# Performance work log

Hardware: AMD Instinct MI355X
Metric: run time of the kernel (lower is better)

The kernel has to match this reference:

```python
import jax, jax.numpy as jnp
import numpy as np

N, DEG, F_IN, F_OUT = 100000, 16, 128, 128
E = N * DEG


def setup_inputs() -> dict:
    key = jax.random.key(0)
    k0, k1, k2, k3 = jax.random.split(key, 4)
    x = jax.random.normal(k0, (N, F_IN), dtype=jnp.float32)
    # ragged neighbor list flattened: each node has DEG neighbors (sorted segment ids)
    neighbor_feats = jax.random.normal(k1, (E, F_IN), dtype=jnp.float32)
    segment_ids = jnp.repeat(jnp.arange(N, dtype=jnp.int32), DEG)
    # nn.Linear(in, out, bias=False) weights, stored [out, in] as in torch
    Wx = jax.random.normal(k2, (F_OUT, F_IN), dtype=jnp.float32) / np.float32(np.sqrt(F_IN))
    Wn = jax.random.normal(k3, (F_OUT, F_IN), dtype=jnp.float32) / np.float32(np.sqrt(F_IN))
    return {"x": x, "neighbor_feats": neighbor_feats, "segment_ids": segment_ids,
            "Wx": Wx, "Wn": Wn}


def reference(x, neighbor_feats, segment_ids, Wx, Wn):
    n_nodes = x.shape[0]
    # MeanAggregator: per-node mean over its neighbor rows (segment mean)
    sums = jax.ops.segment_sum(neighbor_feats, segment_ids, num_segments=n_nodes)
    counts = jax.ops.segment_sum(
        jnp.ones((neighbor_feats.shape[0],), dtype=x.dtype), segment_ids,
        num_segments=n_nodes)
    f = sums / jnp.maximum(counts, 1.0)[:, None]  # [N, F_IN]
    # tranx(x) + trann(f)
    x_out = x @ Wx.T + f @ Wn.T                   # [N, F_OUT]
    # neighbor = [tranx(n) for n in neighbor], flattened
    nb_out = neighbor_feats @ Wx.T                # [E, F_OUT]
    return x_out, nb_out
```

## Files before the change

kernel.cpp:

```cpp
#include <hip/hip_runtime.h>
#include <stdint.h>
#include <stddef.h>

#define N_NODES 100000
#define F_DIM   128
#define DEG     16
#define N_EDGES (N_NODES*DEG)
#define ROWS_PER_TILE 128
#define N_TILES (N_EDGES/ROWS_PER_TILE)
#define NODES_PER_TILE (ROWS_PER_TILE/DEG)
#define GRID_BLOCKS 2500
#define TILES_PER_BLOCK (N_TILES/GRID_BLOCKS)
#define BLOCK_THREADS 256
#define G_STRIDE 132

typedef __bf16 bf16;
typedef __bf16 bf16x8 __attribute__((ext_vector_type(8)));
typedef float  f32x4  __attribute__((ext_vector_type(4)));

__device__ __forceinline__ int swz(int row, int col) {
  return row*128 + (col ^ ((row & 7) << 3));
}

__device__ __forceinline__ bf16x8 cvt8(f32x4 a, f32x4 b) {
  bf16x8 v;
  v[0]=(bf16)a[0]; v[1]=(bf16)a[1]; v[2]=(bf16)a[2]; v[3]=(bf16)a[3];
  v[4]=(bf16)b[0]; v[5]=(bf16)b[1]; v[6]=(bf16)b[2]; v[7]=(bf16)b[3];
  return v;
}

__device__ __forceinline__ bf16x8 load_frag_g(const float* __restrict__ p) {
  f32x4 a = *(const f32x4*)p;
  f32x4 b = *(const f32x4*)(p + 4);
  return cvt8(a, b);
}

__global__ __launch_bounds__(BLOCK_THREADS, 2)
void feattrans_kernel(const float* __restrict__ x,
                      const float* __restrict__ nb,
                      const float* __restrict__ Wx,
                      const float* __restrict__ Wn,
                      float* __restrict__ out)
{
  __shared__ bf16  w_lds[2*128*128];
  __shared__ float g_lds[2][NODES_PER_TILE][G_STRIDE];

  const int tid  = threadIdx.x;
  const int wave = tid >> 6;
  const int lane = tid & 63;
  const int l15  = lane & 15;
  const int lk   = lane >> 4;

  #pragma unroll
  for (int it = 0; it < 16; ++it) {
    int idx = it * BLOCK_THREADS + tid;
    int mat = idx >> 11;
    int rem = idx & 2047;
    int row = rem >> 4;
    int g   = rem & 15;
    const float* src = (mat ? Wn : Wx) + row*128 + g*8;
    bf16x8 v = load_frag_g(src);
    *(bf16x8*)&w_lds[mat*16384 + swz(row, g*8)] = v;
  }
  __syncthreads();

  float* out_x  = out;
  float* out_nb = out + (size_t)N_NODES * F_DIM;

  const int bid = blockIdx.x;

  bf16x8 afr[2][2][4];

  {
    const size_t erow0 = (size_t)bid * ROWS_PER_TILE;
    #pragma unroll
    for (int mt = 0; mt < 2; ++mt)
      #pragma unroll
      for (int ks = 0; ks < 4; ++ks)
        afr[0][mt][ks] = load_frag_g(nb + (erow0 + wave*32 + mt*16 + l15) * F_DIM + ks*32 + lk*8);
  }

  #pragma unroll
  for (int t = 0; t < TILES_PER_BLOCK; ++t) {
    const int cur = t & 1, nxt = cur ^ 1;
    const int tile = bid + t * GRID_BLOCKS;
    const size_t erow0 = (size_t)tile * ROWS_PER_TILE;
    const int nodebase = tile * NODES_PER_TILE;

    int xrow = nodebase + l15;
    if (xrow > N_NODES - 1) xrow = N_NODES - 1;
    bf16x8 xfr[4];
    #pragma unroll
    for (int ks = 0; ks < 4; ++ks)
      xfr[ks] = load_frag_g(x + (size_t)xrow * F_DIM + ks*32 + lk*8);

    f32x4 acc[2][8] = {};
    #pragma unroll
    for (int nt = 0; nt < 8; ++nt) {
      #pragma unroll
      for (int ks = 0; ks < 4; ++ks) {
        bf16x8 bfr = *(bf16x8*)&w_lds[swz(nt*16 + l15, ks*32 + lk*8)];
        acc[0][nt] = __builtin_amdgcn_mfma_f32_16x16x32_bf16(bfr, afr[cur][0][ks], acc[0][nt], 0, 0, 0);
        acc[1][nt] = __builtin_amdgcn_mfma_f32_16x16x32_bf16(bfr, afr[cur][1][ks], acc[1][nt], 0, 0, 0);
      }
    }
    #pragma unroll
    for (int mt = 0; mt < 2; ++mt)
      #pragma unroll
      for (int nt = 0; nt < 8; ++nt)
        *(f32x4*)(out_nb + (erow0 + wave*32 + mt*16 + l15) * F_DIM + nt*16 + lk*4) = acc[mt][nt];

    f32x4 a2[2][8] = {};
    #pragma unroll
    for (int nt = 0; nt < 8; ++nt) {
      #pragma unroll
      for (int ks = 0; ks < 4; ++ks) {
        bf16x8 bfr = *(bf16x8*)&w_lds[16384 + swz(nt*16 + l15, ks*32 + lk*8)];
        a2[0][nt] = __builtin_amdgcn_mfma_f32_16x16x32_bf16(afr[cur][0][ks], bfr, a2[0][nt], 0, 0, 0);
        a2[1][nt] = __builtin_amdgcn_mfma_f32_16x16x32_bf16(afr[cur][1][ks], bfr, a2[1][nt], 0, 0, 0);
      }
    }
    #pragma unroll
    for (int mt = 0; mt < 2; ++mt) {
      const int gnode = 2*wave + mt;
      #pragma unroll
      for (int nt = 0; nt < 8; ++nt) {
        float s = a2[mt][nt][0] + a2[mt][nt][1] + a2[mt][nt][2] + a2[mt][nt][3];
        s += __shfl_xor(s, 16, 64);
        s += __shfl_xor(s, 32, 64);
        s *= (1.0f / DEG);
        if (lk == (nt >> 1))
          g_lds[cur][gnode][nt*16 + l15] = s;
      }
    }

    if (t < TILES_PER_BLOCK - 1) {
      const size_t erowN = erow0 + (size_t)GRID_BLOCKS * ROWS_PER_TILE;
      #pragma unroll
      for (int mt = 0; mt < 2; ++mt)
        #pragma unroll
        for (int ks = 0; ks < 4; ++ks)
          afr[nxt][mt][ks] = load_frag_g(nb + (erowN + wave*32 + mt*16 + l15) * F_DIM + ks*32 + lk*8);
    }

    __syncthreads();

    f32x4 xacc[2] = {};
    #pragma unroll
    for (int j = 0; j < 2; ++j) {
      const int nt = 2*wave + j;
      #pragma unroll
      for (int ks = 0; ks < 4; ++ks) {
        bf16x8 bx = *(bf16x8*)&w_lds[swz(nt*16 + l15, ks*32 + lk*8)];
        xacc[j] = __builtin_amdgcn_mfma_f32_16x16x32_bf16(bx, xfr[ks], xacc[j], 0, 0, 0);
      }
    }
    if (l15 < NODES_PER_TILE) {
      #pragma unroll
      for (int j = 0; j < 2; ++j) {
        const int nt = 2*wave + j;
        f32x4 g4 = *(f32x4*)&g_lds[cur][l15][nt*16 + lk*4];
        f32x4 v  = xacc[j] + g4;
        *(f32x4*)(out_x + (size_t)(nodebase + l15) * F_DIM + nt*16 + lk*4) = v;
      }
    }
  }
}

extern "C" void kernel_launch(void* const* d_in, const int* in_sizes, int n_in,
                              void* d_out, int out_size, void* d_ws, size_t ws_size,
                              hipStream_t stream) {
  const float* x  = (const float*)d_in[0];
  const float* nb = (const float*)d_in[1];
  const float* Wx = (const float*)d_in[3];
  const float* Wn = (const float*)d_in[4];
  float* out = (float*)d_out;

  feattrans_kernel<<<dim3(GRID_BLOCKS), dim3(BLOCK_THREADS), 0, stream>>>(x, nb, Wx, Wn, out);
}
```

Measured before the change: 355.6 us.

## Use 8 waves per block with 16 rows per wave and halved accumulators

Doubles the block to 512 threads so each wave processes 16 edge rows instead of 32, and splits the output-column loop into two halves to cut live accumulator registers. The intent is more resident waves to hide global memory latency in this bandwidth-bound kernel. In exchange, each weight fragment read from LDS now feeds fewer MFMAs, raising LDS traffic, and the LDS footprint still limits how many blocks fit per CU.

```diff
diff --git a/kernel.cpp b/kernel.cpp
--- a/kernel.cpp
+++ b/kernel.cpp
@@ -11,7 +11,7 @@
 #define NODES_PER_TILE (ROWS_PER_TILE/DEG)
 #define GRID_BLOCKS 2500
 #define TILES_PER_BLOCK (N_TILES/GRID_BLOCKS)
-#define BLOCK_THREADS 256
+#define BLOCK_THREADS 512
 #define G_STRIDE 132
 
 typedef __bf16 bf16;
@@ -35,7 +35,7 @@
   return cvt8(a, b);
 }
 
-__global__ __launch_bounds__(BLOCK_THREADS, 2)
+__global__ __launch_bounds__(BLOCK_THREADS, 4)
 void feattrans_kernel(const float* __restrict__ x,
                       const float* __restrict__ nb,
                       const float* __restrict__ Wx,
@@ -52,7 +52,7 @@
   const int lk   = lane >> 4;
 
   #pragma unroll
-  for (int it = 0; it < 16; ++it) {
+  for (int it = 0; it < 8; ++it) {
     int idx = it * BLOCK_THREADS + tid;
     int mat = idx >> 11;
     int rem = idx & 2047;
@@ -69,15 +69,13 @@
 
   const int bid = blockIdx.x;
 
-  bf16x8 afr[2][2][4];
+  bf16x8 afr[2][4];
 
   {
     const size_t erow0 = (size_t)bid * ROWS_PER_TILE;
     #pragma unroll
-    for (int mt = 0; mt < 2; ++mt)
-      #pragma unroll
-      for (int ks = 0; ks < 4; ++ks)
-        afr[0][mt][ks] = load_frag_g(nb + (erow0 + wave*32 + mt*16 + l15) * F_DIM + ks*32 + lk*8);
+    for (int ks = 0; ks < 4; ++ks)
+      afr[0][ks] = load_frag_g(nb + (erow0 + wave*16 + l15) * F_DIM + ks*32 + lk*8);
   }
 
   #pragma unroll
@@ -94,75 +92,68 @@
     for (int ks = 0; ks < 4; ++ks)
       xfr[ks] = load_frag_g(x + (size_t)xrow * F_DIM + ks*32 + lk*8);
 
-    f32x4 acc[2][8] = {};
     #pragma unroll
-    for (int nt = 0; nt < 8; ++nt) {
+    for (int h = 0; h < 2; ++h) {
+      f32x4 acc[4] = {};
       #pragma unroll
-      for (int ks = 0; ks < 4; ++ks) {
-        bf16x8 bfr = *(bf16x8*)&w_lds[swz(nt*16 + l15, ks*32 + lk*8)];
-        acc[0][nt] = __builtin_amdgcn_mfma_f32_16x16x32_bf16(bfr, afr[cur][0][ks], acc[0][nt], 0, 0, 0);
-        acc[1][nt] = __builtin_amdgcn_mfma_f32_16x16x32_bf16(bfr, afr[cur][1][ks], acc[1][nt], 0, 0, 0);
+      for (int q = 0; q < 4; ++q) {
+        const int nt = h*4 + q;
+        #pragma unroll
+        for (int ks = 0; ks < 4; ++ks) {
+          bf16x8 bfr = *(bf16x8*)&w_lds[swz(nt*16 + l15, ks*32 + lk*8)];
+          acc[q] = __builtin_amdgcn_mfma_f32_16x16x32_bf16(bfr, afr[cur][ks], acc[q], 0, 0, 0);
+        }
+      }
+      #pragma unroll
+      for (int q = 0; q < 4; ++q) {
+        const int nt = h*4 + q;
+        *(f32x4*)(out_nb + (erow0 + wave*16 + l15) * F_DIM + nt*16 + lk*4) = acc[q];
       }
     }
+
     #pragma unroll
-    for (int mt = 0; mt < 2; ++mt)
+    for (int h = 0; h < 2; ++h) {
+      f32x4 a2[4] = {};
       #pragma unroll
-      for (int nt = 0; nt < 8; ++nt)
-        *(f32x4*)(out_nb + (erow0 + wave*32 + mt*16 + l15) * F_DIM + nt*16 + lk*4) = acc[mt][nt];
-
-    f32x4 a2[2][8] = {};
-    #pragma unroll
-    for (int nt = 0; nt < 8; ++nt) {
+      for (int q = 0; q < 4; ++q) {
+        const int nt = h*4 + q;
+        #pragma unroll
+        for (int ks = 0; ks < 4; ++ks) {
+          bf16x8 bfr = *(bf16x8*)&w_lds[16384 + swz(nt*16 + l15, ks*32 + lk*8)];
+          a2[q] = __builtin_amdgcn_mfma_f32_16x16x32_bf16(afr[cur][ks], bfr, a2[q], 0, 0, 0);
+        }
+      }
       #pragma unroll
-      for (int ks = 0; ks < 4; ++ks) {
-        bf16x8 bfr = *(bf16x8*)&w_lds[16384 + swz(nt*16 + l15, ks*32 + lk*8)];
-        a2[0][nt] = __builtin_amdgcn_mfma_f32_16x16x32_bf16(afr[cur][0][ks], bfr, a2[0][nt], 0, 0, 0);
-        a2[1][nt] = __builtin_amdgcn_mfma_f32_16x16x32_bf16(afr[cur][1][ks], bfr, a2[1][nt], 0, 0, 0);
-      }
-    }
-    #pragma unroll
-    for (int mt = 0; mt < 2; ++mt) {
-      const int gnode = 2*wave + mt;
-      #pragma unroll
-      for (int nt = 0; nt < 8; ++nt) {
-        float s = a2[mt][nt][0] + a2[mt][nt][1] + a2[mt][nt][2] + a2[mt][nt][3];
+      for (int q = 0; q < 4; ++q) {
+        const int nt = h*4 + q;
+        float s = a2[q][0] + a2[q][1] + a2[q][2] + a2[q][3];
         s += __shfl_xor(s, 16, 64);
         s += __shfl_xor(s, 32, 64);
         s *= (1.0f / DEG);
         if (lk == (nt >> 1))
-          g_lds[cur][gnode][nt*16 + l15] = s;
+          g_lds[cur][wave][nt*16 + l15] = s;
       }
     }
 
     if (t < TILES_PER_BLOCK - 1) {
       const size_t erowN = erow0 + (size_t)GRID_BLOCKS * ROWS_PER_TILE;
       #pragma unroll
-      for (int mt = 0; mt < 2; ++mt)
-        #pragma unroll
-        for (int ks = 0; ks < 4; ++ks)
-          afr[nxt][mt][ks] = load_frag_g(nb + (erowN + wave*32 + mt*16 + l15) * F_DIM + ks*32 + lk*8);
+      for (int ks = 0; ks < 4; ++ks)
+        afr[nxt][ks] = load_frag_g(nb + (erowN + wave*16 + l15) * F_DIM + ks*32 + lk*8);
     }
 
     __syncthreads();
 
-    f32x4 xacc[2] = {};
+    f32x4 xacc = {};
     #pragma unroll
-    for (int j = 0; j < 2; ++j) {
-      const int nt = 2*wave + j;
-      #pragma unroll
-      for (int ks = 0; ks < 4; ++ks) {
-        bf16x8 bx = *(bf16x8*)&w_lds[swz(nt*16 + l15, ks*32 + lk*8)];
-        xacc[j] = __builtin_amdgcn_mfma_f32_16x16x32_bf16(bx, xfr[ks], xacc[j], 0, 0, 0);
-      }
+    for (int ks = 0; ks < 4; ++ks) {
+      bf16x8 bx = *(bf16x8*)&w_lds[swz(wave*16 + l15, ks*32 + lk*8)];
+      xacc = __builtin_amdgcn_mfma_f32_16x16x32_bf16(bx, xfr[ks], xacc, 0, 0, 0);
     }
     if (l15 < NODES_PER_TILE) {
-      #pragma unroll
-      for (int j = 0; j < 2; ++j) {
-        const int nt = 2*wave + j;
-        f32x4 g4 = *(f32x4*)&g_lds[cur][l15][nt*16 + lk*4];
-        f32x4 v  = xacc[j] + g4;
-        *(f32x4*)(out_x + (size_t)(nodebase + l15) * F_DIM + nt*16 + lk*4) = v;
-      }
+      f32x4 g4 = *(f32x4*)&g_lds[cur][l15][wave*16 + lk*4];
+      f32x4 v  = xacc + g4;
+      *(f32x4*)(out_x + (size_t)(nodebase + l15) * F_DIM + wave*16 + lk*4) = v;
     }
   }
 }
```

New measurement: 383.3 us. +7.8%, slower.
